# Optimization experiments

Measured on AMD Instinct MI355X. Metric: run time of the kernel, lower is better.

Reference implementation:

```python
import jax, jax.numpy as jnp
import numpy as np

NUM_BBOX = 2
NUM_CLASSES = 20
NUM_GRID = 7
THR_CONF = 0.5
THR_NMS = 0.3
BATCH = 128


def setup_inputs() -> dict:
    key = jax.random.key(0)
    C = NUM_BBOX * 4 + NUM_BBOX + NUM_CLASSES  # 30
    p = jax.random.normal(key, (BATCH, NUM_GRID, NUM_GRID, C), dtype=jnp.float32)
    return {"p_yolo_ts4": p}


def _decode(p):
    B, S = p.shape[0], p.shape[1]
    sc = NUM_BBOX * 4
    conf = jax.nn.sigmoid(p[..., sc:sc + NUM_BBOX])          # [B,S,S,nb] objectness
    cls = jax.nn.sigmoid(p[..., sc + NUM_BBOX:])             # [B,S,S,nc]
    boxes = p[..., :sc].reshape(B, S, S, NUM_BBOX, 4)
    xy = jax.nn.sigmoid(boxes[..., :2])                      # cell-relative offsets
    col = jnp.arange(S, dtype=p.dtype)
    cx = (xy[..., 0] + col[None, None, :, None]) / NUM_GRID  # + col index (x)
    cy = (xy[..., 1] + col[None, :, None, None]) / NUM_GRID  # + row index (y)
    w, h = boxes[..., 2], boxes[..., 3]                      # raw wh, as in source
    ltrb = jnp.stack([cx - w / 2, cy - h / 2, cx + w / 2, cy + h / 2], axis=-1)
    labels = jnp.argmax(cls, axis=-1) + 1                    # [B,S,S]
    valid = conf > THR_CONF                                  # [B,S,S,nb]
    return ltrb, conf, labels, valid


def _pairwise_iou(b):
    lt = jnp.maximum(b[:, None, :2], b[None, :, :2])
    rb = jnp.minimum(b[:, None, 2:], b[None, :, 2:])
    wh = jnp.clip(rb - lt, 0.0)
    inter = wh[..., 0] * wh[..., 1]
    area = (b[:, 2] - b[:, 0]) * (b[:, 3] - b[:, 1])
    union = area[:, None] + area[None, :] - inter
    return inter / jnp.maximum(union, 1e-9)


def reference(p_yolo_ts4):
    p = p_yolo_ts4
    B, S = p.shape[0], p.shape[1]
    ltrb, conf, labels, valid = _decode(p)
    N = B * S * S * NUM_BBOX
    boxes = ltrb.reshape(N, 4)
    scores = conf.reshape(N)
    labs = jnp.broadcast_to(labels[..., None], (B, S, S, NUM_BBOX)).reshape(N)
    idsb = jnp.broadcast_to(jnp.arange(B)[:, None, None, None], (B, S, S, NUM_BBOX)).reshape(N)
    vmask = valid.reshape(N)
    # sort by score (invalid last); greedy NMS per (batch, label) group
    order = jnp.argsort(jnp.where(vmask, scores, -jnp.inf))[::-1]
    boxes_s = boxes[order]
    scores_s = scores[order]
    labs_s = labs[order]
    idsb_s = idsb[order]
    v_s = vmask[order]
    iou = _pairwise_iou(boxes_s)                              # [N,N]
    same = (idsb_s[:, None] == idsb_s[None, :]) & (labs_s[:, None] == labs_s[None, :])
    later = jnp.arange(N)[None, :] > jnp.arange(N)[:, None]
    sup_mat = (iou > THR_NMS) & same & later & v_s[None, :]

    def body(i, sup):
        keep_i = v_s[i] & jnp.logical_not(sup[i])
        return jnp.where(keep_i, sup | sup_mat[i], sup)

    sup = jax.lax.fori_loop(0, N, body, jnp.zeros((N,), dtype=bool))
    keep = v_s & jnp.logical_not(sup)
    # fixed-shape outputs in descending-score order; `keep` marks surviving boxes
    return idsb_s, boxes_s, labs_s, scores_s, keep
```

## Files before the change

### kernel.cpp

```cpp
#include <hip/hip_runtime.h>
#include <math.h>

#define NBATCH 128
#define S 7
#define NCLS 20
#define CH 30
#define N 12544
#define PERB 98
#define NWORDS 196
#define NBLK 49
#define NCHUNK 16
#define CLENMAX 784
#define MAXK 112
#define THRNMS 0.3

__device__ __forceinline__ float sigf(float x) {
    float e = (float)exp(-(double)x);
    return 1.0f / (1.0f + e);
}

__global__ __launch_bounds__(256) void k_decode(
    const float* __restrict__ p,
    unsigned int* __restrict__ key,
    float* __restrict__ score,
    float* __restrict__ box,
    int* __restrict__ meta,
    unsigned long long* __restrict__ ballots)
{
    int i    = blockIdx.x * 256 + threadIdx.x;
    int lane = threadIdx.x & 63;
    int j    = i & 1;
    int cell = i >> 1;
    int x = cell % S, y = (cell / S) % S, b = cell / (S * S);
    const float* pc = p + cell * CH;

    float tx = pc[j*4+0], ty = pc[j*4+1], tw = pc[j*4+2], th = pc[j*4+3];
    float craw = pc[8 + j];

    int cbase = 10 + j * 10;
    float best = sigf(pc[cbase]); int lab = j * 10;
    #pragma unroll
    for (int c = 1; c < 10; ++c) {
        float v = sigf(pc[cbase + c]);
        if (v > best) { best = v; lab = j * 10 + c; }
    }
    float obest = __shfl_xor(best, 1);
    int   olab  = __shfl_xor(lab, 1);
    float bestA = j ? obest : best;  int labA = j ? olab : lab;
    float bestB = j ? best  : obest; int labB = j ? lab  : olab;
    int label = (bestB > bestA ? labB : labA) + 1;

    float sx = sigf(tx), sy = sigf(ty);
    float cx = (sx + (float)x) / 7.0f;
    float cy = (sy + (float)y) / 7.0f;
    float hw = tw / 2.0f, hh = th / 2.0f;
    float l = cx - hw, t = cy - hh, r = cx + hw, bt = cy + hh;

    float sc = sigf(craw);
    bool valid = sc > 0.5f;

    key[i]   = valid ? __float_as_uint(sc) : 0u;
    score[i] = sc;
    box[i*4+0] = l; box[i*4+1] = t; box[i*4+2] = r; box[i*4+3] = bt;
    meta[i] = (valid ? 0x8000 : 0) | (b << 5) | label;

    unsigned long long vb = __ballot(valid);
    if (lane == 0) ballots[i >> 6] = vb;
}

__global__ __launch_bounds__(256) void k_compact(
    const unsigned long long* __restrict__ ballots,
    const unsigned int* __restrict__ key,
    const float* __restrict__ score,
    const float* __restrict__ box,
    const int* __restrict__ meta,
    unsigned long long* __restrict__ vK,
    unsigned int* __restrict__ vrank,
    unsigned int* __restrict__ nvalid,
    float* __restrict__ out)
{
    __shared__ unsigned int boff[NBLK];
    __shared__ unsigned int nv_sh;
    const int tid = threadIdx.x, lane = tid & 63;

    if ((tid >> 6) == 0) {
        unsigned int c = 0;
        if (lane < NBLK) {
            const unsigned long long* bp = ballots + lane * 4;
            c = __popcll(bp[0]) + __popcll(bp[1]) + __popcll(bp[2]) + __popcll(bp[3]);
        }
        unsigned int v = c;
        #pragma unroll
        for (int d = 1; d < 64; d <<= 1) {
            unsigned int o = __shfl_up(v, d);
            if (lane >= d) v += o;
        }
        if (lane < NBLK) boff[lane] = v - c;
        if (lane == 63) nv_sh = v;
    }
    __syncthreads();

    int i  = blockIdx.x * 256 + tid;
    int wv = tid >> 6;
    int wbase = blockIdx.x * 4;
    unsigned int pre = 0;
    for (int w2 = 0; w2 < wv; ++w2) pre += __popcll(ballots[wbase + w2]);
    unsigned long long myb = ballots[wbase + wv];
    unsigned int wpre = __popcll(myb & ((1ull << lane) - 1ull));
    bool valid = (myb >> lane) & 1ull;
    unsigned int Vexc = boff[blockIdx.x] + pre + wpre;

    if (valid) {
        vK[Vexc] = ((unsigned long long)key[i] << 32) | (unsigned long long)i;
        vrank[Vexc] = 0u;
    } else {
        unsigned int pos = (unsigned int)(N - 1 - i) + Vexc;
        int m = meta[i];
        out[pos] = (float)((m >> 5) & 0x7F);
        ((float4*)(out + N))[pos] = ((const float4*)box)[i];
        out[5*N + pos] = (float)(m & 31);
        out[6*N + pos] = score[i];
        out[7*N + pos] = 0.0f;
    }

    if (blockIdx.x == 0 && tid == 0) nvalid[0] = nv_sh;
}

__global__ __launch_bounds__(256) void k_rankv(
    const unsigned long long* __restrict__ vK,
    const unsigned int* __restrict__ nvalid_p,
    unsigned int* __restrict__ vrank)
{
    __shared__ unsigned long long lk[CLENMAX];
    const unsigned int nv = nvalid_p[0];
    if ((unsigned int)(blockIdx.x * 256) >= nv) return;
    unsigned int clen = (nv + NCHUNK - 1) / NCHUNK;
    unsigned int base = blockIdx.y * clen;
    if (base >= nv) return;
    unsigned int len = (nv - base < clen) ? nv - base : clen;

    for (unsigned int u = threadIdx.x; u < len; u += 256) lk[u] = vK[base + u];
    __syncthreads();

    unsigned int s = blockIdx.x * 256 + threadIdx.x;
    if (s < nv) {
        unsigned long long Ki = vK[s];
        unsigned int cnt = 0;
        for (unsigned int u = 0; u < len; ++u)
            cnt += (lk[u] > Ki) ? 1u : 0u;
        if (cnt) atomicAdd(&vrank[s], cnt);
    }
}

__global__ __launch_bounds__(256) void k_scatnms(
    const unsigned long long* __restrict__ vK,
    const unsigned int* __restrict__ nvalid_p,
    const unsigned int* __restrict__ vrank,
    const float* __restrict__ score,
    const float* __restrict__ box,
    const int* __restrict__ meta,
    float* __restrict__ out)
{
    const int b   = blockIdx.x;
    const int tid = threadIdx.x;
    __shared__ unsigned long long mK[MAXK];
    __shared__ int mslot[MAXK];
    __shared__ unsigned int cnt_sh;
    __shared__ float sbx[MAXK][4];
    __shared__ int   slb[MAXK], spos[MAXK], sup[MAXK];
    __shared__ float ssc[MAXK];

    if (tid == 0) cnt_sh = 0u;
    __syncthreads();

    const unsigned int nv = nvalid_p[0];
    for (unsigned int s = tid; s < nv; s += 256) {
        unsigned long long K = vK[s];
        unsigned int idx = (unsigned int)(K & 0xFFFFFFFFull);
        if ((int)(idx / PERB) == b) {
            unsigned int m = atomicAdd(&cnt_sh, 1u);
            mK[m] = K; mslot[m] = (int)s;
        }
    }
    __syncthreads();
    const int kb = (int)cnt_sh;

    if (tid < kb) {
        unsigned long long Kt = mK[tid];
        int rk = 0;
        for (int u = 0; u < kb; ++u) rk += (mK[u] > Kt) ? 1 : 0;
        unsigned int idx = (unsigned int)(Kt & 0xFFFFFFFFull);
        float4 b4 = ((const float4*)box)[idx];
        sbx[rk][0] = b4.x; sbx[rk][1] = b4.y; sbx[rk][2] = b4.z; sbx[rk][3] = b4.w;
        slb[rk]  = meta[idx] & 31;
        ssc[rk]  = score[idx];
        spos[rk] = (int)vrank[mslot[tid]];
        sup[rk]  = 0;
    }
    __syncthreads();

    for (int i = 0; i < kb; ++i) {
        __syncthreads();
        if (sup[i]) continue;
        float li = sbx[i][0], ti = sbx[i][1], ri = sbx[i][2], bi = sbx[i][3];
        float areai = (ri - li) * (bi - ti);
        int labi = slb[i];
        int jj = tid;
        if (jj > i && jj < kb && slb[jj] == labi) {
            float lj = sbx[jj][0], tj = sbx[jj][1], rj = sbx[jj][2], bj = sbx[jj][3];
            float lt0 = fmaxf(li, lj), lt1 = fmaxf(ti, tj);
            float rb0 = fminf(ri, rj), rb1 = fminf(bi, bj);
            float w = rb0 - lt0; if (w < 0.0f) w = 0.0f;
            float h = rb1 - lt1; if (h < 0.0f) h = 0.0f;
            float inter = w * h;
            float areaj = (rj - lj) * (bj - tj);
            float uni = areai + areaj - inter;
            double iou = (double)inter / fmax((double)uni, 1e-9);
            if (iou > THRNMS) sup[jj] = 1;
        }
    }
    __syncthreads();

    if (tid < kb) {
        int pos = spos[tid];
        out[pos] = (float)b;
        ((float4*)(out + N))[pos] =
            make_float4(sbx[tid][0], sbx[tid][1], sbx[tid][2], sbx[tid][3]);
        out[5*N + pos] = (float)slb[tid];
        out[6*N + pos] = ssc[tid];
        out[7*N + pos] = sup[tid] ? 0.0f : 1.0f;
    }
}

extern "C" void kernel_launch(void* const* d_in, const int* in_sizes, int n_in,
                              void* d_out, int out_size, void* d_ws, size_t ws_size,
                              hipStream_t stream)
{
    const float* p = (const float*)d_in[0];
    float* out = (float*)d_out;

    char* w = (char*)d_ws;
    float* box          = (float*)w;                      w += (size_t)N * 16;
    unsigned int* key   = (unsigned int*)w;               w += (size_t)N * 4;
    float* score        = (float*)w;                      w += (size_t)N * 4;
    int* meta           = (int*)w;                        w += (size_t)N * 4;
    unsigned long long* ballots = (unsigned long long*)w; w += (size_t)NWORDS * 8;
    unsigned long long* vK      = (unsigned long long*)w; w += (size_t)N * 8;
    unsigned int* vrank = (unsigned int*)w;               w += (size_t)N * 4;
    unsigned int* nvalid= (unsigned int*)w;               w += 4;

    k_decode <<<dim3(NBLK),         dim3(256), 0, stream>>>(p, key, score, box, meta, ballots);
    k_compact<<<dim3(NBLK),         dim3(256), 0, stream>>>(ballots, key, score, box, meta,
                                                            vK, vrank, nvalid, out);
    k_rankv  <<<dim3(NBLK, NCHUNK), dim3(256), 0, stream>>>(vK, nvalid, vrank);
    k_scatnms<<<dim3(NBATCH),       dim3(256), 0, stream>>>(vK, nvalid, vrank,
                                                            score, box, meta, out);
}
```

Before: 85.43 us.

## Fuse decode, compaction and ranking into two kernels with chunked rank partials

Replaces the four-kernel pipeline (decode, compact, rank, scatter+NMS) with two kernels. The first recomputes confidence directly from the input per chunk and counts, for each box, the valid boxes ranked ahead of it (for invalid boxes, valid boxes with lower index), writing per-chunk partial counts. The second redoes the full per-batch decode, sums the partials to find each box's output position, and runs NMS. This removes two launches, the intermediate workspace traffic and the global atomics. In exchange it repeats sigmoid work and uses a dense N-by-chunk partial array.

```diff
diff --git a/kernel.cpp b/kernel.cpp
--- a/kernel.cpp
+++ b/kernel.cpp
@@ -3,15 +3,11 @@
 
 #define NBATCH 128
 #define S 7
-#define NCLS 20
 #define CH 30
 #define N 12544
 #define PERB 98
-#define NWORDS 196
-#define NBLK 49
+#define CLEN 784
 #define NCHUNK 16
-#define CLENMAX 784
-#define MAXK 112
 #define THRNMS 0.3
 
 __device__ __forceinline__ float sigf(float x) {
@@ -19,183 +15,137 @@
     return 1.0f / (1.0f + e);
 }
 
-__global__ __launch_bounds__(256) void k_decode(
-    const float* __restrict__ p,
-    unsigned int* __restrict__ key,
-    float* __restrict__ score,
-    float* __restrict__ box,
-    int* __restrict__ meta,
-    unsigned long long* __restrict__ ballots)
-{
-    int i    = blockIdx.x * 256 + threadIdx.x;
-    int lane = threadIdx.x & 63;
-    int j    = i & 1;
-    int cell = i >> 1;
-    int x = cell % S, y = (cell / S) % S, b = cell / (S * S);
-    const float* pc = p + cell * CH;
-
-    float tx = pc[j*4+0], ty = pc[j*4+1], tw = pc[j*4+2], th = pc[j*4+3];
-    float craw = pc[8 + j];
-
-    int cbase = 10 + j * 10;
-    float best = sigf(pc[cbase]); int lab = j * 10;
-    #pragma unroll
-    for (int c = 1; c < 10; ++c) {
-        float v = sigf(pc[cbase + c]);
-        if (v > best) { best = v; lab = j * 10 + c; }
-    }
-    float obest = __shfl_xor(best, 1);
-    int   olab  = __shfl_xor(lab, 1);
-    float bestA = j ? obest : best;  int labA = j ? olab : lab;
-    float bestB = j ? best  : obest; int labB = j ? lab  : olab;
-    int label = (bestB > bestA ? labB : labA) + 1;
-
-    float sx = sigf(tx), sy = sigf(ty);
-    float cx = (sx + (float)x) / 7.0f;
-    float cy = (sy + (float)y) / 7.0f;
-    float hw = tw / 2.0f, hh = th / 2.0f;
-    float l = cx - hw, t = cy - hh, r = cx + hw, bt = cy + hh;
-
-    float sc = sigf(craw);
-    bool valid = sc > 0.5f;
-
-    key[i]   = valid ? __float_as_uint(sc) : 0u;
-    score[i] = sc;
-    box[i*4+0] = l; box[i*4+1] = t; box[i*4+2] = r; box[i*4+3] = bt;
-    meta[i] = (valid ? 0x8000 : 0) | (b << 5) | label;
-
-    unsigned long long vb = __ballot(valid);
-    if (lane == 0) ballots[i >> 6] = vb;
+__device__ __forceinline__ float confraw(const float* __restrict__ p, int i) {
+    return p[(i >> 1) * CH + 8 + (i & 1)];
 }
 
-__global__ __launch_bounds__(256) void k_compact(
-    const unsigned long long* __restrict__ ballots,
-    const unsigned int* __restrict__ key,
-    const float* __restrict__ score,
-    const float* __restrict__ box,
-    const int* __restrict__ meta,
-    unsigned long long* __restrict__ vK,
-    unsigned int* __restrict__ vrank,
-    unsigned int* __restrict__ nvalid,
-    float* __restrict__ out)
+__global__ __launch_bounds__(256) void k_rank(
+    const float* __restrict__ p,
+    unsigned int* __restrict__ vpart)
 {
-    __shared__ unsigned int boff[NBLK];
-    __shared__ unsigned int nv_sh;
-    const int tid = threadIdx.x, lane = tid & 63;
+    __shared__ unsigned long long lk[CLEN];
+    __shared__ unsigned int cnt_sh;
+    const int tid = threadIdx.x;
+    const int rb = blockIdx.x, ch = blockIdx.y;
 
-    if ((tid >> 6) == 0) {
-        unsigned int c = 0;
-        if (lane < NBLK) {
-            const unsigned long long* bp = ballots + lane * 4;
-            c = __popcll(bp[0]) + __popcll(bp[1]) + __popcll(bp[2]) + __popcll(bp[3]);
+    if (tid == 0) cnt_sh = 0u;
+    __syncthreads();
+
+    for (int u = tid; u < CLEN; u += 256) {
+        int jg = ch * CLEN + u;
+        float craw = confraw(p, jg);
+        if (craw > 0.0f) {
+            float sc = sigf(craw);
+            if (sc > 0.5f) {
+                unsigned int m = atomicAdd(&cnt_sh, 1u);
+                lk[m] = ((unsigned long long)__float_as_uint(sc) << 32)
+                        | (unsigned long long)(unsigned int)jg;
+            }
         }
-        unsigned int v = c;
-        #pragma unroll
-        for (int d = 1; d < 64; d <<= 1) {
-            unsigned int o = __shfl_up(v, d);
-            if (lane >= d) v += o;
-        }
-        if (lane < NBLK) boff[lane] = v - c;
-        if (lane == 63) nv_sh = v;
     }
     __syncthreads();
+    const unsigned int len = cnt_sh;
 
-    int i  = blockIdx.x * 256 + tid;
-    int wv = tid >> 6;
-    int wbase = blockIdx.x * 4;
-    unsigned int pre = 0;
-    for (int w2 = 0; w2 < wv; ++w2) pre += __popcll(ballots[wbase + w2]);
-    unsigned long long myb = ballots[wbase + wv];
-    unsigned int wpre = __popcll(myb & ((1ull << lane) - 1ull));
-    bool valid = (myb >> lane) & 1ull;
-    unsigned int Vexc = boff[blockIdx.x] + pre + wpre;
-
-    if (valid) {
-        vK[Vexc] = ((unsigned long long)key[i] << 32) | (unsigned long long)i;
-        vrank[Vexc] = 0u;
-    } else {
-        unsigned int pos = (unsigned int)(N - 1 - i) + Vexc;
-        int m = meta[i];
-        out[pos] = (float)((m >> 5) & 0x7F);
-        ((float4*)(out + N))[pos] = ((const float4*)box)[i];
-        out[5*N + pos] = (float)(m & 31);
-        out[6*N + pos] = score[i];
-        out[7*N + pos] = 0.0f;
+    const int i = rb * 256 + tid;
+    float crawi = confraw(p, i);
+    bool validi = false;
+    unsigned long long Ki = 0ull;
+    if (crawi > 0.0f) {
+        float sc = sigf(crawi);
+        if (sc > 0.5f) {
+            validi = true;
+            Ki = ((unsigned long long)__float_as_uint(sc) << 32)
+                 | (unsigned long long)(unsigned int)i;
+        }
     }
 
-    if (blockIdx.x == 0 && tid == 0) nvalid[0] = nv_sh;
+    const unsigned int ui = (unsigned int)i;
+    unsigned int cnt = 0;
+    for (unsigned int u = 0; u < len; ++u) {
+        unsigned long long K = lk[u];
+        unsigned int c1 = (K > Ki) ? 1u : 0u;
+        unsigned int c2 = ((unsigned int)K < ui) ? 1u : 0u;
+        cnt += validi ? c1 : c2;
+    }
+    vpart[ch * N + i] = cnt;
 }
 
-__global__ __launch_bounds__(256) void k_rankv(
-    const unsigned long long* __restrict__ vK,
-    const unsigned int* __restrict__ nvalid_p,
-    unsigned int* __restrict__ vrank)
-{
-    __shared__ unsigned long long lk[CLENMAX];
-    const unsigned int nv = nvalid_p[0];
-    if ((unsigned int)(blockIdx.x * 256) >= nv) return;
-    unsigned int clen = (nv + NCHUNK - 1) / NCHUNK;
-    unsigned int base = blockIdx.y * clen;
-    if (base >= nv) return;
-    unsigned int len = (nv - base < clen) ? nv - base : clen;
-
-    for (unsigned int u = threadIdx.x; u < len; u += 256) lk[u] = vK[base + u];
-    __syncthreads();
-
-    unsigned int s = blockIdx.x * 256 + threadIdx.x;
-    if (s < nv) {
-        unsigned long long Ki = vK[s];
-        unsigned int cnt = 0;
-        for (unsigned int u = 0; u < len; ++u)
-            cnt += (lk[u] > Ki) ? 1u : 0u;
-        if (cnt) atomicAdd(&vrank[s], cnt);
-    }
-}
-
-__global__ __launch_bounds__(256) void k_scatnms(
-    const unsigned long long* __restrict__ vK,
-    const unsigned int* __restrict__ nvalid_p,
-    const unsigned int* __restrict__ vrank,
-    const float* __restrict__ score,
-    const float* __restrict__ box,
-    const int* __restrict__ meta,
+__global__ __launch_bounds__(256) void k_finish(
+    const float* __restrict__ p,
+    const unsigned int* __restrict__ vpart,
     float* __restrict__ out)
 {
     const int b   = blockIdx.x;
     const int tid = threadIdx.x;
-    __shared__ unsigned long long mK[MAXK];
-    __shared__ int mslot[MAXK];
-    __shared__ unsigned int cnt_sh;
-    __shared__ float sbx[MAXK][4];
-    __shared__ int   slb[MAXK], spos[MAXK], sup[MAXK];
-    __shared__ float ssc[MAXK];
+    __shared__ int   lab49[49];
+    __shared__ float bxa[PERB][4];
+    __shared__ float sca[PERB];
+    __shared__ unsigned long long Ka[PERB];
+    __shared__ unsigned int posa[PERB];
+    __shared__ int   srk[PERB];
+    __shared__ float sbx[PERB][4];
+    __shared__ int   slb[PERB], sup[PERB];
+    __shared__ unsigned int kb_sh;
 
-    if (tid == 0) cnt_sh = 0u;
-    __syncthreads();
+    if (tid == 0) kb_sh = 0u;
 
-    const unsigned int nv = nvalid_p[0];
-    for (unsigned int s = tid; s < nv; s += 256) {
-        unsigned long long K = vK[s];
-        unsigned int idx = (unsigned int)(K & 0xFFFFFFFFull);
-        if ((int)(idx / PERB) == b) {
-            unsigned int m = atomicAdd(&cnt_sh, 1u);
-            mK[m] = K; mslot[m] = (int)s;
+    if (tid < PERB) {
+        int c = tid >> 1, half = tid & 1;
+        const float* pc = p + (b * 49 + c) * CH;
+        int cbase = 10 + half * 10;
+        float best = sigf(pc[cbase]); int lab = half * 10;
+        #pragma unroll
+        for (int q = 1; q < 10; ++q) {
+            float v = sigf(pc[cbase + q]);
+            if (v > best) { best = v; lab = half * 10 + q; }
         }
+        float obest = __shfl_xor(best, 1);
+        int   olab  = __shfl_xor(lab, 1);
+        float bestA = half ? obest : best;  int labA = half ? olab : lab;
+        float bestB = half ? best  : obest; int labB = half ? lab  : olab;
+        if (half == 0) lab49[c] = (bestB > bestA ? labB : labA) + 1;
+    }
+
+    if (tid < PERB) {
+        int i = b * PERB + tid;
+        int j = tid & 1, c = tid >> 1;
+        const float* pc = p + (b * 49 + c) * CH;
+        float tx = pc[j*4+0], ty = pc[j*4+1], tw = pc[j*4+2], th = pc[j*4+3];
+        float craw = pc[8 + j];
+
+        float sx = sigf(tx), sy = sigf(ty);
+        int xg = c % S, yg = c / S;
+        float cx = (sx + (float)xg) / 7.0f;
+        float cy = (sy + (float)yg) / 7.0f;
+        float hw = tw / 2.0f, hh = th / 2.0f;
+        bxa[tid][0] = cx - hw; bxa[tid][1] = cy - hh;
+        bxa[tid][2] = cx + hw; bxa[tid][3] = cy + hh;
+
+        float sc = sigf(craw);
+        sca[tid] = sc;
+        bool valid = sc > 0.5f;
+        Ka[tid] = valid ? (((unsigned long long)__float_as_uint(sc) << 32)
+                           | (unsigned long long)(unsigned int)i)
+                        : 0ull;
+
+        unsigned int acc = 0;
+        #pragma unroll
+        for (int chn = 0; chn < NCHUNK; ++chn) acc += vpart[chn * N + i];
+        posa[tid] = valid ? acc : (unsigned int)(N - 1 - i) + acc;
+        if (valid) atomicAdd(&kb_sh, 1u);
     }
     __syncthreads();
-    const int kb = (int)cnt_sh;
+    const int kb = (int)kb_sh;
 
-    if (tid < kb) {
-        unsigned long long Kt = mK[tid];
+    if (tid < PERB && Ka[tid] != 0ull) {
+        unsigned long long Kt = Ka[tid];
         int rk = 0;
-        for (int u = 0; u < kb; ++u) rk += (mK[u] > Kt) ? 1 : 0;
-        unsigned int idx = (unsigned int)(Kt & 0xFFFFFFFFull);
-        float4 b4 = ((const float4*)box)[idx];
-        sbx[rk][0] = b4.x; sbx[rk][1] = b4.y; sbx[rk][2] = b4.z; sbx[rk][3] = b4.w;
-        slb[rk]  = meta[idx] & 31;
-        ssc[rk]  = score[idx];
-        spos[rk] = (int)vrank[mslot[tid]];
-        sup[rk]  = 0;
+        for (int u = 0; u < PERB; ++u) rk += (Ka[u] > Kt) ? 1 : 0;
+        srk[tid] = rk;
+        sbx[rk][0] = bxa[tid][0]; sbx[rk][1] = bxa[tid][1];
+        sbx[rk][2] = bxa[tid][2]; sbx[rk][3] = bxa[tid][3];
+        slb[rk] = lab49[tid >> 1];
+        sup[rk] = 0;
     }
     __syncthreads();
 
@@ -221,14 +171,15 @@
     }
     __syncthreads();
 
-    if (tid < kb) {
-        int pos = spos[tid];
+    if (tid < PERB) {
+        unsigned int pos = posa[tid];
+        bool valid = Ka[tid] != 0ull;
         out[pos] = (float)b;
         ((float4*)(out + N))[pos] =
-            make_float4(sbx[tid][0], sbx[tid][1], sbx[tid][2], sbx[tid][3]);
-        out[5*N + pos] = (float)slb[tid];
-        out[6*N + pos] = ssc[tid];
-        out[7*N + pos] = sup[tid] ? 0.0f : 1.0f;
+            make_float4(bxa[tid][0], bxa[tid][1], bxa[tid][2], bxa[tid][3]);
+        out[5*N + pos] = (float)lab49[tid >> 1];
+        out[6*N + pos] = sca[tid];
+        out[7*N + pos] = (valid && !sup[srk[tid]]) ? 1.0f : 0.0f;
     }
 }
 
@@ -238,21 +189,8 @@
 {
     const float* p = (const float*)d_in[0];
     float* out = (float*)d_out;
+    unsigned int* vpart = (unsigned int*)d_ws;
 
-    char* w = (char*)d_ws;
-    float* box          = (float*)w;                      w += (size_t)N * 16;
-    unsigned int* key   = (unsigned int*)w;               w += (size_t)N * 4;
-    float* score        = (float*)w;                      w += (size_t)N * 4;
-    int* meta           = (int*)w;                        w += (size_t)N * 4;
-    unsigned long long* ballots = (unsigned long long*)w; w += (size_t)NWORDS * 8;
-    unsigned long long* vK      = (unsigned long long*)w; w += (size_t)N * 8;
-    unsigned int* vrank = (unsigned int*)w;               w += (size_t)N * 4;
-    unsigned int* nvalid= (unsigned int*)w;               w += 4;
-
-    k_decode <<<dim3(NBLK),         dim3(256), 0, stream>>>(p, key, score, box, meta, ballots);
-    k_compact<<<dim3(NBLK),         dim3(256), 0, stream>>>(ballots, key, score, box, meta,
-                                                            vK, vrank, nvalid, out);
-    k_rankv  <<<dim3(NBLK, NCHUNK), dim3(256), 0, stream>>>(vK, nvalid, vrank);
-    k_scatnms<<<dim3(NBATCH),       dim3(256), 0, stream>>>(vK, nvalid, vrank,
-                                                            score, box, meta, out);
+    k_rank  <<<dim3(49, NCHUNK), dim3(256), 0, stream>>>(p, vpart);
+    k_finish<<<dim3(NBATCH),     dim3(256), 0, stream>>>(p, vpart, out);
 }
```

Result: slower. 89.98 us (+5.3%).
